# Kernel optimization log

Measured on AMD Instinct MI355X. Metric: run time of the kernel, lower is better.

## Reference

```python
import jax, jax.numpy as jnp
from jax import lax
import numpy as np

NUM_GRIDS = (40, 36, 24, 16, 12)
B, C = 4, 256
SMPL_OUT, CATE_OUT = 157, 1  # 24*6 pose + 10 shape + 3 cam; num_classes-1
SIZES = ((200, 200), (100, 100), (50, 50), (25, 25), (13, 13))


def setup_inputs():
    key = jax.random.key(0)
    ks = jax.random.split(key, 16)
    inp = {}
    for i, (h, w) in enumerate(SIZES):
        inp['feat%d' % i] = jax.random.normal(ks[i], (B, C, h, w), jnp.float32)
    def W(k, shape):
        return jax.random.normal(k, shape, jnp.float32) * 0.02
    inp['smpl_w0'] = W(ks[5], (C, C + 2, 3, 3)); inp['smpl_b0'] = jnp.zeros((C,), jnp.float32)
    inp['smpl_w'] = W(ks[6], (3, C, C, 3, 3)); inp['smpl_b'] = jnp.zeros((3, C), jnp.float32)
    inp['cate_w0'] = W(ks[7], (C, C, 3, 3)); inp['cate_b0'] = jnp.zeros((C,), jnp.float32)
    inp['cate_w'] = W(ks[8], (3, C, C, 3, 3)); inp['cate_b'] = jnp.zeros((3, C), jnp.float32)
    inp['cate_head_w'] = W(ks[9], (CATE_OUT, C, 3, 3)); inp['cate_head_b'] = jnp.zeros((CATE_OUT,), jnp.float32)
    inp['smpl_head_w'] = W(ks[10], (SMPL_OUT, C, 1, 1)); inp['smpl_head_b'] = jnp.zeros((SMPL_OUT,), jnp.float32)
    inp['smpl_init'] = W(ks[11], (SMPL_OUT,))  # stands in for init_contrep/shape/cam buffer
    return inp


def conv2d(x, w, b, pad):
    y = lax.conv_general_dilated(x, w, (1, 1), [(pad, pad), (pad, pad)],
                                 dimension_numbers=('NCHW', 'OIHW', 'NCHW'))
    return y + b[None, :, None, None]


def resize_ac(x, oh, ow):
    # bilinear resize, align_corners=True (matches F.interpolate(..., align_corners=True))
    H, W = x.shape[-2], x.shape[-1]
    ys = jnp.linspace(0.0, H - 1.0, oh)
    xs = jnp.linspace(0.0, W - 1.0, ow)
    y0 = jnp.floor(ys).astype(jnp.int32); y1 = jnp.minimum(y0 + 1, H - 1)
    x0 = jnp.floor(xs).astype(jnp.int32); x1 = jnp.minimum(x0 + 1, W - 1)
    wy = (ys - y0)[:, None]; wx = xs - x0
    r0, r1 = x[..., y0, :], x[..., y1, :]
    top = r0[..., x0] * (1 - wx) + r0[..., x1] * wx
    bot = r1[..., x0] * (1 - wx) + r1[..., x1] * wx
    return top * (1 - wy) + bot * wy


def points_nms(heat):
    # max_pool2d(kernel=2, stride=1, pad=1) -> (H+1, W+1); compare on [:-1, :-1]
    hmax = lax.reduce_window(heat, -jnp.inf, lax.max, (1, 1, 2, 2), (1, 1, 1, 1),
                             [(0, 0), (0, 0), (1, 1), (1, 1)])[:, :, :-1, :-1]
    return heat * (hmax == heat).astype(heat.dtype)


def _forward(feats, p):
    # split_feats: downsample P2 by 0.5, upsample P6 to P5 size (both align_corners bilinear)
    f0 = resize_ac(feats[0], feats[0].shape[-2] // 2, feats[0].shape[-1] // 2)
    f4 = resize_ac(feats[4], feats[3].shape[-2], feats[3].shape[-1])
    new_feats = (f0, feats[1], feats[2], feats[3], f4)
    smpl_outs, cate_outs = [], []
    for idx, x in enumerate(new_feats):
        g = NUM_GRIDS[idx]
        b, _, h, w = x.shape
        xr = jnp.linspace(-1.0, 1.0, w); yr = jnp.linspace(-1.0, 1.0, h)
        yy, xx = jnp.meshgrid(yr, xr, indexing='ij')
        coord = jnp.broadcast_to(jnp.stack([xx, yy])[None], (b, 2, h, w))  # CoordConv
        smpl_feat = resize_ac(jnp.concatenate([x, coord], axis=1), g, g)
        cate_feat = resize_ac(x, g, g)
        smpl_feat = jax.nn.relu(conv2d(smpl_feat, p['smpl_w0'], p['smpl_b0'], 1))
        cate_feat = jax.nn.relu(conv2d(cate_feat, p['cate_w0'], p['cate_b0'], 1))
        for i in range(3):  # remaining stacked convs (weights shared across levels)
            smpl_feat = jax.nn.relu(conv2d(smpl_feat, p['smpl_w'][i], p['smpl_b'][i], 1))
            cate_feat = jax.nn.relu(conv2d(cate_feat, p['cate_w'][i], p['cate_b'][i], 1))
        cate_pred = conv2d(cate_feat, p['cate_head_w'], p['cate_head_b'], 1)
        smpl_pred = conv2d(smpl_feat, p['smpl_head_w'], p['smpl_head_b'], 0) \
                    + p['smpl_init'][None, :, None, None]
        # eval=True branch: points-NMS on sigmoid heatmap, NHWC permute
        cate_pred = points_nms(jax.nn.sigmoid(cate_pred)).transpose(0, 2, 3, 1)
        smpl_pred = smpl_pred.transpose(0, 2, 3, 1)
        smpl_outs.append(smpl_pred); cate_outs.append(cate_pred)
    return tuple(smpl_outs) + tuple(cate_outs)


def reference(feat0, feat1, feat2, feat3, feat4, smpl_w0, smpl_b0, smpl_w, smpl_b,
              cate_w0, cate_b0, cate_w, cate_b, cate_head_w, cate_head_b,
              smpl_head_w, smpl_head_b, smpl_init):
    p = dict(smpl_w0=smpl_w0, smpl_b0=smpl_b0, smpl_w=smpl_w, smpl_b=smpl_b,
             cate_w0=cate_w0, cate_b0=cate_b0, cate_w=cate_w, cate_b=cate_b,
             cate_head_w=cate_head_w, cate_head_b=cate_head_b,
             smpl_head_w=smpl_head_w, smpl_head_b=smpl_head_b, smpl_init=smpl_init)
    return _forward((feat0, feat1, feat2, feat3, feat4), p)
```

## Files before the change

kernel.cpp:

```cpp
#include <hip/hip_runtime.h>
#include <math.h>
#include <stdint.h>

#define NLEV 5
#define PPT 17616

typedef __attribute__((ext_vector_type(8))) __bf16 bf16x8;
typedef __attribute__((ext_vector_type(4))) float f32x4;
typedef unsigned int u32;
typedef unsigned short u16;

__device__ __forceinline__ u32 f2bf(float f) {
  u32 u = __builtin_bit_cast(u32, f);
  return (u + 0x7FFFu + ((u >> 16) & 1u)) >> 16;
}
__device__ __forceinline__ u32 packSplit(float v) {
  u32 hi = f2bf(v);
  float fhi = __builtin_bit_cast(float, hi << 16);
  u32 lo = f2bf(v - fhi);
  return hi | (lo << 16);
}
__device__ __forceinline__ float unpackSum(u32 w) {
  return __builtin_bit_cast(float, w << 16) +
         __builtin_bit_cast(float, w & 0xFFFF0000u);
}


struct PrepDesc {
  const float* src[8];
  int Cin[8];
  int CB[8];
  int dstOff[8];
};

__global__ __launch_bounds__(256) void prep_weights(PrepDesc pd, u16* __restrict__ wHi,
                                                    u16* __restrict__ wLo) {
  int cfg = blockIdx.y;
  int CB = pd.CB[cfg];
  int KS = CB * 9;
  int total = KS * 8192;
  int didx = blockIdx.x * 256 + threadIdx.x;
  if (didx >= total) return;
  int j = didx & 7;
  int lane = (didx >> 3) & 63;
  int wco = (didx >> 9) & 1;
  int f = (didx >> 10) & 1;
  int rest = didx >> 11;
  int ks = rest % KS;
  int coT = rest / KS;
  int cb = ks / 9;
  int tap = ks - cb * 9;
  int ci = cb * 32 + ((lane >> 4) << 3) + j;
  int co = coT * 64 + wco * 32 + f * 16 + (lane & 15);
  int Cin = pd.Cin[cfg];
  float v = 0.f;
  if (ci < Cin) v = pd.src[cfg][((size_t)co * Cin + ci) * 9 + tap];
  u32 hi = f2bf(v);
  float fhi = __builtin_bit_cast(float, hi << 16);
  u32 lo = f2bf(v - fhi);
  wHi[pd.dstOff[cfg] + didx] = (u16)hi;
  wLo[pd.dstOff[cfg] + didx] = (u16)lo;
}

struct BuildDesc {
  const float* src[NLEV];
  int H[NLEV];
  int mid[NLEV];
  int P[NLEV];
  int g[NLEV];
  int padOff[NLEV];
};

__device__ __forceinline__ float bsample(const float* __restrict__ pl, int H, int W,
                                         float fy, float fx) {
  int y0 = (int)floorf(fy);
  int y1 = min(y0 + 1, H - 1);
  float wy = fy - (float)y0;
  int x0 = (int)floorf(fx);
  int x1 = min(x0 + 1, W - 1);
  float wx = fx - (float)x0;
  const float* r0 = pl + (size_t)y0 * W;
  const float* r1 = pl + (size_t)y1 * W;
  float top = r0[x0] * (1.f - wx) + r0[x1] * wx;
  float bot = r1[x0] * (1.f - wx) + r1[x1] * wx;
// ... 35 lines not shown
      float wy = fym - (float)y0;
      int x0 = (int)floorf(fxm);
      int x1 = min(x0 + 1, midw - 1);
      float wx = fxm - (float)x0;
      float sy0 = (float)y0 * (float)(H - 1) / (float)(midh - 1);
      float sy1 = (float)y1 * (float)(H - 1) / (float)(midh - 1);
      float sx0 = (float)x0 * (float)(W - 1) / (float)(midw - 1);
      float sx1 = (float)x1 * (float)(W - 1) / (float)(midw - 1);
      float v00 = bsample(pl, H, W, sy0, sx0);
      float v01 = bsample(pl, H, W, sy0, sx1);
      float v10 = bsample(pl, H, W, sy1, sx0);
      float v11 = bsample(pl, H, W, sy1, sx1);
      float top = v00 * (1.f - wx) + v01 * wx;
      float bot = v10 * (1.f - wx) + v11 * wx;
      val = top * (1.f - wy) + bot * wy;
    }
  }
  int gp2 = g + 2;
  int hpos = bd.padOff[l] + b * gp2 * gp2 + (i + 1) * gp2 + (j + 1);
  dst[((size_t)(c >> 3) * PPT + hpos) * 8 + (c & 7)] = packSplit(val);
}

struct ConvDesc {
  int tileStart[NLEV + 1];
  int padOff[NLEV];
  int g[NLEV];
};

#define HPX 240

__global__ __launch_bounds__(256) void conv_mfma(
    const u32* __restrict__ actIn, const u16* __restrict__ wHi,
    const u16* __restrict__ wLo, const float* __restrict__ bias,
    u32* __restrict__ actOut, ConvDesc d, int CB) {
  const int bid = blockIdx.x;
  const int xcd = bid & 7;
  const int i6 = bid >> 3;
  const int coT = i6 & 3;
  const int tile = xcd + (i6 >> 2) * 8;
  const int NT = d.tileStart[NLEV];
  if (tile >= NT) return;

  int l = 0;
#pragma unroll
  for (int i = 1; i < NLEV; i++)
    if (tile >= d.tileStart[i]) l = i;
  const int g = d.g[l];
  const int gp2 = g + 2;
  const int hp2 = gp2 * gp2;
  const int gg = g * g;
  const int padOff = d.padOff[l];
  const int t = threadIdx.x;
  const int lane = t & 63;
  const int wv = t >> 6;
  const int wco = wv & 1, wp = wv >> 1;
  const int KS = CB * 9;
  const int ptile = (tile - d.tileStart[l]) * 64;

  int b0 = ptile / gg;
  int pr0 = ptile - b0 * gg;
  int y0p = pr0 / g;
  int x0p = pr0 - y0p * g;
  const int h0 = padOff + b0 * hp2 + (y0p + 1) * gp2 + (x0p + 1) - gp2 - 1;

  const int pF0 = ptile + wp * 32 + (lane & 15);
  int bF = pF0 / gg;
  int prF = pF0 - bF * gg;
  int yF = prF / g;
  int xF = prF - yF * g;
  const int hF0 = padOff + bF * hp2 + (yF + 1) * gp2 + (xF + 1);
  int pF1 = pF0 + 16;
  int bF1 = pF1 / gg;
  int prF1 = pF1 - bF1 * gg;
  int yF1 = prF1 / g;
  int xF1 = prF1 - yF1 * g;
  const int hF1 = padOff + bF1 * hp2 + (yF1 + 1) * gp2 + (xF1 + 1);

  const int kb = lane >> 4;
  const int base0 = (hF0 - h0) * 4 + kb * (2 * HPX * 4);
  const int base1 = (hF1 - h0) * 4 + kb * (2 * HPX * 4);

  __shared__ u32 halo[4 * 2 * HPX * 4];

  const int sgr = t >> 6;
  const int spx = t & 63;

  f32x4 acc00 = {0.f, 0.f, 0.f, 0.f}, acc01 = {0.f, 0.f, 0.f, 0.f};
  f32x4 acc10 = {0.f, 0.f, 0.f, 0.f}, acc11 = {0.f, 0.f, 0.f, 0.f};

  const size_t wbase =
      (size_t)coT * KS * 2048 + (size_t)wco * 512 + (size_t)lane * 8;
  bf16x8 ah0 = *(const bf16x8*)(wHi + wbase);
  bf16x8 ah1 = *(const bf16x8*)(wHi + wbase + 1024);
  bf16x8 al0 = *(const bf16x8*)(wLo + wbase);
  bf16x8 al1 = *(const bf16x8*)(wLo + wbase + 1024);

  for (int cb = 0; cb < CB; ++cb) {
    __syncthreads();
    {
      int gr = cb * 4 + sgr;
      const u32* srcp = actIn + ((size_t)gr * PPT + h0 + spx) * 8;
#pragma unroll
      for (int i = 0; i < 4; i++) {
        int idx = i * 64 + spx;
        uint4 a = *(const uint4*)(srcp + (size_t)i * 512);
        uint4 b2 = *(const uint4*)(srcp + (size_t)i * 512 + 4);
        if (idx < HPX) {
          *(uint4*)(halo + sgr * (2 * HPX * 4) + idx * 4) = a;
          *(uint4*)(halo + sgr * (2 * HPX * 4) + HPX * 4 + idx * 4) = b2;
        }
      }
    }
    __syncthreads();

#pragma unroll
    for (int tap = 0; tap < 9; ++tap) {
      const int ks = cb * 9 + tap;
      bf16x8 ah0n, ah1n, al0n, al1n;
      const bool have = (ks + 1) < KS;
      if (have) {
        size_t wo = wbase + (size_t)(ks + 1) * 2048;
        ah0n = *(const bf16x8*)(wHi + wo);
        ah1n = *(const bf16x8*)(wHi + wo + 1024);
        al0n = *(const bf16x8*)(wLo + wo);
        al1n = *(const bf16x8*)(wLo + wo + 1024);
      }
      const int toff = (tap / 3 - 1) * gp2 + (tap % 3) - 1;
      const u32* hp0 = halo + base0 + toff * 4;
      uint4 q0 = *(const uint4*)hp0;
      uint4 q1 = *(const uint4*)(hp0 + HPX * 4);
      const u32* hp1 = halo + base1 + toff * 4;
      uint4 r0 = *(const uint4*)hp1;
      uint4 r1 = *(const uint4*)(hp1 + HPX * 4);

      bf16x8 bh0, bl0, bh1, bl1;
      {
        uint4 hq, lq;
        hq.x = __builtin_amdgcn_perm(q0.y, q0.x, 0x05040100u);
        hq.y = __builtin_amdgcn_perm(q0.w, q0.z, 0x05040100u);
        hq.z = __builtin_amdgcn_perm(q1.y, q1.x, 0x05040100u);
        hq.w = __builtin_amdgcn_perm(q1.w, q1.z, 0x05040100u);
        lq.x = __builtin_amdgcn_perm(q0.y, q0.x, 0x07060302u);
        lq.y = __builtin_amdgcn_perm(q0.w, q0.z, 0x07060302u);
        lq.z = __builtin_amdgcn_perm(q1.y, q1.x, 0x07060302u);
        lq.w = __builtin_amdgcn_perm(q1.w, q1.z, 0x07060302u);
        bh0 = __builtin_bit_cast(bf16x8, hq);
        bl0 = __builtin_bit_cast(bf16x8, lq);
        hq.x = __builtin_amdgcn_perm(r0.y, r0.x, 0x05040100u);
        hq.y = __builtin_amdgcn_perm(r0.w, r0.z, 0x05040100u);
        hq.z = __builtin_amdgcn_perm(r1.y, r1.x, 0x05040100u);
        hq.w = __builtin_amdgcn_perm(r1.w, r1.z, 0x05040100u);
        lq.x = __builtin_amdgcn_perm(r0.y, r0.x, 0x07060302u);
        lq.y = __builtin_amdgcn_perm(r0.w, r0.z, 0x07060302u);
        lq.z = __builtin_amdgcn_perm(r1.y, r1.x, 0x07060302u);
        lq.w = __builtin_amdgcn_perm(r1.w, r1.z, 0x07060302u);
        bh1 = __builtin_bit_cast(bf16x8, hq);
        bl1 = __builtin_bit_cast(bf16x8, lq);
      }

      acc00 = __builtin_amdgcn_mfma_f32_16x16x32_bf16(ah0, bh0, acc00, 0, 0, 0);
      acc00 = __builtin_amdgcn_mfma_f32_16x16x32_bf16(ah0, bl0, acc00, 0, 0, 0);
      acc00 = __builtin_amdgcn_mfma_f32_16x16x32_bf16(al0, bh0, acc00, 0, 0, 0);
      acc01 = __builtin_amdgcn_mfma_f32_16x16x32_bf16(ah0, bh1, acc01, 0, 0, 0);
      acc01 = __builtin_amdgcn_mfma_f32_16x16x32_bf16(ah0, bl1, acc01, 0, 0, 0);
      acc01 = __builtin_amdgcn_mfma_f32_16x16x32_bf16(al0, bh1, acc01, 0, 0, 0);
      acc10 = __builtin_amdgcn_mfma_f32_16x16x32_bf16(ah1, bh0, acc10, 0, 0, 0);
      acc10 = __builtin_amdgcn_mfma_f32_16x16x32_bf16(ah1, bl0, acc10, 0, 0, 0);
      acc10 = __builtin_amdgcn_mfma_f32_16x16x32_bf16(al1, bh0, acc10, 0, 0, 0);
      acc11 = __builtin_amdgcn_mfma_f32_16x16x32_bf16(ah1, bh1, acc11, 0, 0, 0);
      acc11 = __builtin_amdgcn_mfma_f32_16x16x32_bf16(ah1, bl1, acc11, 0, 0, 0);
      acc11 = __builtin_amdgcn_mfma_f32_16x16x32_bf16(al1, bh1, acc11, 0, 0, 0);
      if (have) {
        ah0 = ah0n;
        ah1 = ah1n;
        al0 = al0n;
        al1 = al1n;
      }
    }
  }

  int obase[2];
#pragma unroll
  for (int fp = 0; fp < 2; ++fp) {
    int po = ptile + wp * 32 + fp * 16 + (lane & 15);
    int bb = po / gg;
    int prr = po - bb * gg;
    int yy = prr / g;
    int xx = prr - yy * g;
    obase[fp] = padOff + bb * hp2 + (yy + 1) * gp2 + (xx + 1);
  }
  const int coBase = coT * 64 + wco * 32 + ((lane >> 4) << 2);
  float4 bA = *(const float4*)(bias + coBase);
  float4 bB = *(const float4*)(bias + coBase + 16);
  const size_t rowA = (size_t)(coBase >> 3) * PPT;
  const size_t rowB = (size_t)((coBase + 16) >> 3) * PPT;
  const int sub = coBase & 7;
  uint4 s;
  s.x = packSplit(fmaxf(acc00[0] + bA.x, 0.f));
  s.y = packSplit(fmaxf(acc00[1] + bA.y, 0.f));
  s.z = packSplit(fmaxf(acc00[2] + bA.z, 0.f));
  s.w = packSplit(fmaxf(acc00[3] + bA.w, 0.f));
  *(uint4*)(actOut + (rowA + obase[0]) * 8 + sub) = s;
  s.x = packSplit(fmaxf(acc01[0] + bA.x, 0.f));
  s.y = packSplit(fmaxf(acc01[1] + bA.y, 0.f));
  s.z = packSplit(fmaxf(acc01[2] + bA.z, 0.f));
  s.w = packSplit(fmaxf(acc01[3] + bA.w, 0.f));
  *(uint4*)(actOut + (rowA + obase[1]) * 8 + sub) = s;
  s.x = packSplit(fmaxf(acc10[0] + bB.x, 0.f));
  s.y = packSplit(fmaxf(acc10[1] + bB.y, 0.f));
  s.z = packSplit(fmaxf(acc10[2] + bB.z, 0.f));
  s.w = packSplit(fmaxf(acc10[3] + bB.w, 0.f));
  *(uint4*)(actOut + (rowB + obase[0]) * 8 + sub) = s;
  s.x = packSplit(fmaxf(acc11[0] + bB.x, 0.f));
  s.y = packSplit(fmaxf(acc11[1] + bB.y, 0.f));
  s.z = packSplit(fmaxf(acc11[2] + bB.z, 0.f));
  s.w = packSplit(fmaxf(acc11[3] + bB.w, 0.f));
  *(uint4*)(actOut + (rowB + obase[1]) * 8 + sub) = s;
}

struct HeadDesc {
  int tileStart[NLEV + 1];
  int padOff[NLEV];
  int g[NLEV];
  int outOff[NLEV];
};

__global__ __launch_bounds__(256) void head1x1(
    const u32* __restrict__ actIn, const float* __restrict__ w,
    const float* __restrict__ bias, const float* __restrict__ bias2,
    float* __restrict__ outB, HeadDesc d) {
  int bx = blockIdx.x;
  int l = 0;
#pragma unroll
  for (int i = 1; i < NLEV; i++)
    if (bx >= d.tileStart[i]) l = i;
  const int g = d.g[l];
  const int gp2 = g + 2, hp2 = gp2 * gp2, gg = g * g;
  const int t = threadIdx.x;
  const int ptile = (bx - d.tileStart[l]) * 64;
  const int pp = t & 63;
  int p = ptile + pp;
  int b = p / gg, pr = p - b * gg, y = pr / g, x = pr - y * g;
  const int hbase = d.padOff[l] + b * hp2 + (y + 1) * gp2 + (x + 1);
  const int co_tile = blockIdx.y * 64;
  __shared__ float As[32][68];
  __shared__ float Bs[32][68];
  const int tx = t & 15, ty = t >> 4;
  const int akk = t & 31, aco = t >> 5;
  const int kg = t >> 6;
  float acc[4][4];
#pragma unroll
  for (int i = 0; i < 4; i++)
#pragma unroll
    for (int j = 0; j < 4; j++) acc[i][j] = 0.f;

  for (int k0 = 0; k0 < 256; k0 += 32) {
#pragma unroll
    for (int i = 0; i < 8; i++) {
      int co = i * 8 + aco;
      int coG = co_tile + co;
      As[akk][co] = (coG < 157) ? w[(size_t)coG * 256 + k0 + akk] : 0.f;
    }
    {
      const u32* src = actIn + (((size_t)(k0 >> 3) + kg) * PPT + hbase) * 8;
#pragma unroll
      for (int j = 0; j < 8; j++) Bs[kg * 8 + j][pp] = unpackSum(src[j]);
    }
    __syncthreads();
#pragma unroll
    for (int kk = 0; kk < 32; kk++) {
      float4 a4 = *reinterpret_cast<const float4*>(&As[kk][ty * 4]);
      float4 b4 = *reinterpret_cast<const float4*>(&Bs[kk][tx * 4]);
      float av[4] = {a4.x, a4.y, a4.z, a4.w};
      float bv[4] = {b4.x, b4.y, b4.z, b4.w};
#pragma unroll
      for (int i = 0; i < 4; i++)
#pragma unroll
        for (int j = 0; j < 4; j++) acc[i][j] = fmaf(av[i], bv[j], acc[i][j]);
    }
    __syncthreads();
  }
  const int co0 = co_tile + ty * 4;
#pragma unroll
  for (int i = 0; i < 4; i++) {
    int co = co0 + i;
    if (co < 157) {
      float bb = bias[co] + bias2[co];
#pragma unroll
      for (int j = 0; j < 4; j++) {
        int pg = ptile + tx * 4 + j;
        outB[d.outOff[l] + (size_t)pg * 157 + co] = acc[i][j] + bb;
      }
    }
  }
}

struct CHDesc {
  int tileStart[NLEV + 1];
  int padOff[NLEV];
  int g[NLEV];
  int outOff[NLEV];
};

__global__ __launch_bounds__(256) void cate_head_all(
    const u32* __restrict__ actIn, const float* __restrict__ w,
    const float* __restrict__ bias, float* __restrict__ heat, CHDesc d) {
  int tile = blockIdx.x;
  int l = 0;
#pragma unroll
  for (int i = 1; i < NLEV; i++)
    if (tile >= d.tileStart[i]) l = i;
  const int g = d.g[l];
  const int gp2 = g + 2, hp2 = gp2 * gp2, gg = g * g;
  const int t = threadIdx.x;
  const int ps = t & 63;
  const int cw = t >> 6;
  const int ptile = (tile - d.tileStart[l]) * 64;
  int p = ptile + ps;
  int b = p / gg, pr = p - b * gg, y = pr / g, x = pr - y * g;
  const int hbase = d.padOff[l] + b * hp2 + (y + 1) * gp2 + (x + 1);

  __shared__ float ws[32][9][8];
  for (int i = t; i < 2304; i += 256) {
    int ci = i / 9, tap = i - ci * 9;
    ws[ci >> 3][tap][ci & 7] = w[i];
  }
  __syncthreads();

  float s = 0.f;
  for (int gr = cw; gr < 32; gr += 4) {
    const u32* bp = actIn + ((size_t)gr * PPT + hbase) * 8;
#pragma unroll
    for (int tap = 0; tap < 9; tap++) {
      const int toff = (tap / 3 - 1) * gp2 + (tap % 3) - 1;
      uint4 q0 = *(const uint4*)(bp + (ptrdiff_t)toff * 8);
      uint4 q1 = *(const uint4*)(bp + (ptrdiff_t)toff * 8 + 4);
      const float* wp = ws[gr][tap];
      s += unpackSum(q0.x) * wp[0] + unpackSum(q0.y) * wp[1] +
           unpackSum(q0.z) * wp[2] + unpackSum(q0.w) * wp[3] +
           unpackSum(q1.x) * wp[4] + unpackSum(q1.y) * wp[5] +
// ... 40 lines not shown
                              void* d_out, int out_size, void* d_ws, size_t ws_size,
                              hipStream_t stream) {
  const float* feat[5];
  for (int i = 0; i < 5; i++) feat[i] = (const float*)d_in[i];
  const float* smpl_w0 = (const float*)d_in[5];
  const float* smpl_b0 = (const float*)d_in[6];
  const float* smpl_w = (const float*)d_in[7];
  const float* smpl_b = (const float*)d_in[8];
  const float* cate_w0 = (const float*)d_in[9];
  const float* cate_b0 = (const float*)d_in[10];
  const float* cate_w = (const float*)d_in[11];
  const float* cate_b = (const float*)d_in[12];
  const float* cate_head_w = (const float*)d_in[13];
  const float* cate_head_b = (const float*)d_in[14];
  const float* smpl_head_w = (const float*)d_in[15];
  const float* smpl_head_b = (const float*)d_in[16];
  const float* smpl_init = (const float*)d_in[17];
  float* out = (float*)d_out;

  static const int GR[5] = {40, 36, 24, 16, 12};
  static const int SH[5] = {200, 100, 50, 25, 13};
  static const int MIDW[5] = {100, 0, 0, 0, 25};

  int P[5], cumP[6], tS[6], padOff[5];
  cumP[0] = 0;
  tS[0] = 0;
  int po = 0;
  for (int l = 0; l < 5; l++) {
    P[l] = 4 * GR[l] * GR[l];
    cumP[l + 1] = cumP[l] + P[l];
    tS[l + 1] = tS[l] + P[l] / 64;
    padOff[l] = po;
    po += 4 * (GR[l] + 2) * (GR[l] + 2);
  }

  int smpl_off[5], cate_off[5];
  {
    int off = 0;
    for (int l = 0; l < 5; l++) {
      smpl_off[l] = off;
      off += P[l] * 157;
    }
    for (int l = 0; l < 5; l++) {
      cate_off[l] = off;
      off += P[l];
    }
  }

  u32* bufA = (u32*)d_ws;
  u32* bufB = bufA + (size_t)33 * PPT * 8;
  u32* bufC = bufB + (size_t)32 * PPT * 8;
  float* heat = (float*)(bufC + (size_t)32 * PPT * 8);
  const size_t WTOT = (size_t)(81 + 7 * 72) * 8192;
  u16* wHi = (u16*)(heat + 15488);
  u16* wLo = wHi + WTOT;
  const size_t ACT_BYTES = (size_t)(33 + 32 + 32) * PPT * 8 * 4 + 15488 * 4;

  hipMemsetAsync(d_ws, 0, ACT_BYTES, stream);

  PrepDesc pd;
  const size_t LSTR = (size_t)256 * 256 * 9;
  pd.src[0] = smpl_w0;  pd.Cin[0] = 258;  pd.CB[0] = 9;
  pd.src[1] = smpl_w;   pd.Cin[1] = 256;  pd.CB[1] = 8;
  pd.src[2] = smpl_w + LSTR;     pd.Cin[2] = 256; pd.CB[2] = 8;
  pd.src[3] = smpl_w + 2 * LSTR; pd.Cin[3] = 256; pd.CB[3] = 8;
  pd.src[4] = cate_w0;  pd.Cin[4] = 256;  pd.CB[4] = 8;
  pd.src[5] = cate_w;   pd.Cin[5] = 256;  pd.CB[5] = 8;
  pd.src[6] = cate_w + LSTR;     pd.Cin[6] = 256; pd.CB[6] = 8;
  pd.src[7] = cate_w + 2 * LSTR; pd.Cin[7] = 256; pd.CB[7] = 8;
  {
    int off = 0;
    for (int i = 0; i < 8; i++) {
      pd.dstOff[i] = off;
      off += pd.CB[i] * 9 * 8192;
    }
  }
  hipLaunchKernelGGL(prep_weights, dim3(81 * 32, 8), dim3(256), 0, stream, pd, wHi,
                     wLo);

  BuildDesc bd;
  for (int l = 0; l < 5; l++) {
    bd.src[l] = feat[l];
    bd.H[l] = SH[l];
    bd.mid[l] = MIDW[l];
    bd.P[l] = P[l];
    bd.g[l] = GR[l];
    bd.padOff[l] = padOff[l];
  }
  hipLaunchKernelGGL(build_all, dim3((258 * P[0] + 255) / 256, 5), dim3(256), 0,
                     stream, bd, bufA);

  ConvDesc cd;
  HeadDesc hd;
  CHDesc chd;
  SmallDesc nd;
  for (int i = 0; i <= 5; i++) {
    cd.tileStart[i] = tS[i];
    hd.tileStart[i] = tS[i];
    chd.tileStart[i] = tS[i];
  }
  for (int l = 0; l < 5; l++) {
    cd.padOff[l] = padOff[l];
    cd.g[l] = GR[l];
    hd.padOff[l] = padOff[l];
    hd.g[l] = GR[l];
    hd.outOff[l] = smpl_off[l];
    chd.padOff[l] = padOff[l];
    chd.g[l] = GR[l];
    chd.outOff[l] = cumP[l];
    nd.P[l] = P[l];
    nd.g[l] = GR[l];
    nd.inOff[l] = cumP[l];
    nd.outOff[l] = cate_off[l];
  }

  const int NT = tS[5];
  const int CGRID = 8 * 124;
  hipLaunchKernelGGL(conv_mfma, dim3(CGRID), dim3(256), 0, stream, bufA,
                     wHi + pd.dstOff[0], wLo + pd.dstOff[0], smpl_b0, bufB, cd, 9);
  hipLaunchKernelGGL(conv_mfma, dim3(CGRID), dim3(256), 0, stream, bufB,
                     wHi + pd.dstOff[1], wLo + pd.dstOff[1], smpl_b + 0, bufC, cd, 8);
  hipLaunchKernelGGL(conv_mfma, dim3(CGRID), dim3(256), 0, stream, bufC,
                     wHi + pd.dstOff[2], wLo + pd.dstOff[2], smpl_b + 256, bufB, cd,
                     8);
  hipLaunchKernelGGL(conv_mfma, dim3(CGRID), dim3(256), 0, stream, bufB,
                     wHi + pd.dstOff[3], wLo + pd.dstOff[3], smpl_b + 512, bufC, cd,
                     8);
  hipLaunchKernelGGL(head1x1, dim3(NT, 3), dim3(256), 0, stream, bufC, smpl_head_w,
                     smpl_head_b, smpl_init, out, hd);
  hipLaunchKernelGGL(conv_mfma, dim3(CGRID), dim3(256), 0, stream, bufA,
                     wHi + pd.dstOff[4], wLo + pd.dstOff[4], cate_b0, bufB, cd, 8);
  hipLaunchKernelGGL(conv_mfma, dim3(CGRID), dim3(256), 0, stream, bufB,
                     wHi + pd.dstOff[5], wLo + pd.dstOff[5], cate_b + 0, bufC, cd, 8);
  hipLaunchKernelGGL(conv_mfma, dim3(CGRID), dim3(256), 0, stream, bufC,
                     wHi + pd.dstOff[6], wLo + pd.dstOff[6], cate_b + 256, bufB, cd,
                     8);
  hipLaunchKernelGGL(conv_mfma, dim3(CGRID), dim3(256), 0, stream, bufB,
                     wHi + pd.dstOff[7], wLo + pd.dstOff[7], cate_b + 512, bufC, cd,
                     8);
  hipLaunchKernelGGL(cate_head_all, dim3(NT), dim3(256), 0, stream, bufC,
                     cate_head_w, cate_head_b, heat, chd);
  hipLaunchKernelGGL(nms_all, dim3((P[0] + 255) / 256, 5), dim3(256), 0, stream,
                     heat, out, nd);
  (void)in_sizes;
  (void)n_in;
  (void)out_size;
  (void)ws_size;
}
```

Baseline: 607.8 us.

## Merge smpl/cate conv towers per launch, widen pixel tiles, MFMA 1x1 head

Each conv launch now runs both the smpl and cate towers, with the tower picked by block index, so eight conv launches become four larger ones. Pixel tiles grow from 64 to 128 per block with four fragments per wave, and the hi/lo split permutation moves into the halo staging step so each tap reads bf16 operands straight from LDS. The 1x1 smpl head moves from a scalar FMA GEMM to MFMA with pre-split weights. The full-buffer memset is replaced by a kernel that zeroes only halo borders. The larger tiles raise register and LDS use and add tail masking for partial tiles.

```diff
diff --git a/kernel.cpp b/kernel.cpp
--- a/kernel.cpp
+++ b/kernel.cpp
@@ -4,11 +4,14 @@
 
 #define NLEV 5
 #define PPT 17616
+#define HPX 320
 
 typedef __attribute__((ext_vector_type(8))) __bf16 bf16x8;
 typedef __attribute__((ext_vector_type(4))) float f32x4;
 typedef unsigned int u32;
 typedef unsigned short u16;
+
+#define MFMA16 __builtin_amdgcn_mfma_f32_16x16x32_bf16
 
 __device__ __forceinline__ u32 f2bf(float f) {
   u32 u = __builtin_bit_cast(u32, f);
@@ -24,21 +27,36 @@
   return __builtin_bit_cast(float, w << 16) +
          __builtin_bit_cast(float, w & 0xFFFF0000u);
 }
+__device__ __forceinline__ void splitPerm(const uint4& a, const uint4& b, uint4& hq,
+                                          uint4& lq) {
+  hq.x = __builtin_amdgcn_perm(a.y, a.x, 0x05040100u);
+  hq.y = __builtin_amdgcn_perm(a.w, a.z, 0x05040100u);
+  hq.z = __builtin_amdgcn_perm(b.y, b.x, 0x05040100u);
+  hq.w = __builtin_amdgcn_perm(b.w, b.z, 0x05040100u);
+  lq.x = __builtin_amdgcn_perm(a.y, a.x, 0x07060302u);
+  lq.y = __builtin_amdgcn_perm(a.w, a.z, 0x07060302u);
+  lq.z = __builtin_amdgcn_perm(b.y, b.x, 0x07060302u);
+  lq.w = __builtin_amdgcn_perm(b.w, b.z, 0x07060302u);
+}
 
 
 struct PrepDesc {
-  const float* src[8];
-  int Cin[8];
-  int CB[8];
-  int dstOff[8];
+  const float* src[9];
+  int Cin[9];
+  int Cout[9];
+  int CB[9];
+  int TAPS[9];
+  int nCoT[9];
+  int dstOff[9];
 };
 
 __global__ __launch_bounds__(256) void prep_weights(PrepDesc pd, u16* __restrict__ wHi,
                                                     u16* __restrict__ wLo) {
   int cfg = blockIdx.y;
   int CB = pd.CB[cfg];
-  int KS = CB * 9;
-  int total = KS * 8192;
+  int TAPS = pd.TAPS[cfg];
+  int KS = CB * TAPS;
+  int total = KS * 2048 * pd.nCoT[cfg];
   int didx = blockIdx.x * 256 + threadIdx.x;
   if (didx >= total) return;
   int j = didx & 7;
@@ -48,18 +66,43 @@
   int rest = didx >> 11;
   int ks = rest % KS;
   int coT = rest / KS;
-  int cb = ks / 9;
-  int tap = ks - cb * 9;
+  int cb = ks / TAPS;
+  int tap = ks - cb * TAPS;
   int ci = cb * 32 + ((lane >> 4) << 3) + j;
   int co = coT * 64 + wco * 32 + f * 16 + (lane & 15);
-  int Cin = pd.Cin[cfg];
   float v = 0.f;
-  if (ci < Cin) v = pd.src[cfg][((size_t)co * Cin + ci) * 9 + tap];
+  if (ci < pd.Cin[cfg] && co < pd.Cout[cfg])
+    v = pd.src[cfg][((size_t)co * pd.Cin[cfg] + ci) * TAPS + tap];
   u32 hi = f2bf(v);
   float fhi = __builtin_bit_cast(float, hi << 16);
   u32 lo = f2bf(v - fhi);
   wHi[pd.dstOff[cfg] + didx] = (u16)hi;
   wLo[pd.dstOff[cfg] + didx] = (u16)lo;
+}
+
+struct ZeroDesc {
+  int padOff[NLEV];
+  int g[NLEV];
+};
+
+__global__ __launch_bounds__(256) void halo_zero(u32* __restrict__ base, ZeroDesc zd) {
+  int px = blockIdx.x * 256 + threadIdx.x;
+  if (px >= PPT) return;
+  int l = 0;
+#pragma unroll
+  for (int i = 1; i < NLEV; i++)
+    if (px >= zd.padOff[i]) l = i;
+  int g = zd.g[l], gp2 = g + 2, hp2 = gp2 * gp2;
+  int local = px - zd.padOff[l];
+  int b = local / hp2;
+  int rem = local - b * hp2;
+  int yy = rem / gp2, xx = rem - yy * gp2;
+  if (yy >= 1 && yy <= g && xx >= 1 && xx <= g) return;
+  int r = blockIdx.y;
+  uint4 z = {0u, 0u, 0u, 0u};
+  u32* p = base + ((size_t)r * PPT + px) * 8;
+  *(uint4*)p = z;
+  *(uint4*)(p + 4) = z;
 }
 
 struct BuildDesc {
@@ -141,93 +184,104 @@
 }
 
 struct ConvDesc {
-  int tileStart[NLEV + 1];
+  int tS[NLEV + 1];
   int padOff[NLEV];
   int g[NLEV];
+  int P[NLEV];
 };
 
-#define HPX 240
-
 __global__ __launch_bounds__(256) void conv_mfma(
-    const u32* __restrict__ actIn, const u16* __restrict__ wHi,
-    const u16* __restrict__ wLo, const float* __restrict__ bias,
-    u32* __restrict__ actOut, ConvDesc d, int CB) {
+    const u32* __restrict__ inS, const u32* __restrict__ inC,
+    const u16* __restrict__ wHiB, const u16* __restrict__ wLoB, int wOffS,
+    int wOffC, const float* __restrict__ bS, const float* __restrict__ bC,
+    u32* __restrict__ outS, u32* __restrict__ outC, ConvDesc d, int CBS, int CBC) {
   const int bid = blockIdx.x;
   const int xcd = bid & 7;
   const int i6 = bid >> 3;
-  const int coT = i6 & 3;
-  const int tile = xcd + (i6 >> 2) * 8;
-  const int NT = d.tileStart[NLEV];
-  if (tile >= NT) return;
+  const int tower = i6 & 1;
+  const int coT = (i6 >> 1) & 3;
+  const int tile = xcd + (i6 >> 3) * 8;
+  if (tile >= d.tS[NLEV]) return;
+
+  const u32* __restrict__ actIn = tower ? inC : inS;
+  u32* __restrict__ actOut = tower ? outC : outS;
+  const u16* __restrict__ wH = wHiB + (tower ? wOffC : wOffS);
+  const u16* __restrict__ wL = wLoB + (tower ? wOffC : wOffS);
+  const float* __restrict__ bias = tower ? bC : bS;
+  const int CB = tower ? CBC : CBS;
+  const int KS = CB * 9;
 
   int l = 0;
 #pragma unroll
   for (int i = 1; i < NLEV; i++)
-    if (tile >= d.tileStart[i]) l = i;
+    if (tile >= d.tS[i]) l = i;
   const int g = d.g[l];
-  const int gp2 = g + 2;
-  const int hp2 = gp2 * gp2;
-  const int gg = g * g;
+  const int gp2 = g + 2, hp2 = gp2 * gp2, gg = g * g;
   const int padOff = d.padOff[l];
+  const int Pl = d.P[l];
+  const int ptile = (tile - d.tS[l]) * 128;
+
   const int t = threadIdx.x;
   const int lane = t & 63;
   const int wv = t >> 6;
   const int wco = wv & 1, wp = wv >> 1;
-  const int KS = CB * 9;
-  const int ptile = (tile - d.tileStart[l]) * 64;
-
-  int b0 = ptile / gg;
-  int pr0 = ptile - b0 * gg;
-  int y0p = pr0 / g;
-  int x0p = pr0 - y0p * g;
-  const int h0 = padOff + b0 * hp2 + (y0p + 1) * gp2 + (x0p + 1) - gp2 - 1;
-
-  const int pF0 = ptile + wp * 32 + (lane & 15);
-  int bF = pF0 / gg;
-  int prF = pF0 - bF * gg;
-  int yF = prF / g;
-  int xF = prF - yF * g;
-  const int hF0 = padOff + bF * hp2 + (yF + 1) * gp2 + (xF + 1);
-  int pF1 = pF0 + 16;
-  int bF1 = pF1 / gg;
-  int prF1 = pF1 - bF1 * gg;
-  int yF1 = prF1 / g;
-  int xF1 = prF1 - yF1 * g;
-  const int hF1 = padOff + bF1 * hp2 + (yF1 + 1) * gp2 + (xF1 + 1);
-
   const int kb = lane >> 4;
-  const int base0 = (hF0 - h0) * 4 + kb * (2 * HPX * 4);
-  const int base1 = (hF1 - h0) * 4 + kb * (2 * HPX * 4);
+  const int sgr = wv;
+  const int spx = lane;
+
+  int h0;
+  {
+    int b0 = ptile / gg, pr0 = ptile - b0 * gg;
+    int y0 = pr0 / g, x0 = pr0 - y0 * g;
+    h0 = padOff + b0 * hp2 + (y0 + 1) * gp2 + (x0 + 1) - gp2 - 1;
+  }
+
+  int hRel[4], ob[4];
+  bool vst[4];
+#pragma unroll
+  for (int fi = 0; fi < 4; fi++) {
+    int pb = ptile + wp * 64 + fi * 16;
+    vst[fi] = pb < Pl;
+    int pf = pb + (lane & 15);
+    if (pf >= Pl) pf = Pl - 1;
+    int b = pf / gg, pr = pf - b * gg;
+    int y = pr / g, x = pr - y * g;
+    int h = padOff + b * hp2 + (y + 1) * gp2 + (x + 1);
+    hRel[fi] = h - h0;
+    ob[fi] = h;
+  }
 
   __shared__ u32 halo[4 * 2 * HPX * 4];
 
-  const int sgr = t >> 6;
-  const int spx = t & 63;
-
-  f32x4 acc00 = {0.f, 0.f, 0.f, 0.f}, acc01 = {0.f, 0.f, 0.f, 0.f};
-  f32x4 acc10 = {0.f, 0.f, 0.f, 0.f}, acc11 = {0.f, 0.f, 0.f, 0.f};
+  f32x4 acc[2][4];
+#pragma unroll
+  for (int c = 0; c < 2; c++)
+#pragma unroll
+    for (int fi = 0; fi < 4; fi++) acc[c][fi] = (f32x4){0.f, 0.f, 0.f, 0.f};
 
   const size_t wbase =
       (size_t)coT * KS * 2048 + (size_t)wco * 512 + (size_t)lane * 8;
-  bf16x8 ah0 = *(const bf16x8*)(wHi + wbase);
-  bf16x8 ah1 = *(const bf16x8*)(wHi + wbase + 1024);
-  bf16x8 al0 = *(const bf16x8*)(wLo + wbase);
-  bf16x8 al1 = *(const bf16x8*)(wLo + wbase + 1024);
+  bf16x8 ah0 = *(const bf16x8*)(wH + wbase);
+  bf16x8 ah1 = *(const bf16x8*)(wH + wbase + 1024);
+  bf16x8 al0 = *(const bf16x8*)(wL + wbase);
+  bf16x8 al1 = *(const bf16x8*)(wL + wbase + 1024);
 
   for (int cb = 0; cb < CB; ++cb) {
     __syncthreads();
     {
-      int gr = cb * 4 + sgr;
-      const u32* srcp = actIn + ((size_t)gr * PPT + h0 + spx) * 8;
-#pragma unroll
-      for (int i = 0; i < 4; i++) {
-        int idx = i * 64 + spx;
-        uint4 a = *(const uint4*)(srcp + (size_t)i * 512);
-        uint4 b2 = *(const uint4*)(srcp + (size_t)i * 512 + 4);
-        if (idx < HPX) {
-          *(uint4*)(halo + sgr * (2 * HPX * 4) + idx * 4) = a;
-          *(uint4*)(halo + sgr * (2 * HPX * 4) + HPX * 4 + idx * 4) = b2;
-        }
+      const int gr = cb * 4 + sgr;
+      const u32* srcp = actIn + ((size_t)gr * PPT + h0) * 8;
+      u32* dhi = halo + sgr * (2 * HPX * 4);
+      u32* dlo = dhi + HPX * 4;
+#pragma unroll
+      for (int i = 0; i < 5; i++) {
+        int px = i * 64 + spx;
+        uint4 a = *(const uint4*)(srcp + (size_t)px * 8);
+        uint4 b2 = *(const uint4*)(srcp + (size_t)px * 8 + 4);
+        uint4 hq, lq;
+        splitPerm(a, b2, hq, lq);
+        *(uint4*)(dhi + px * 4) = hq;
+        *(uint4*)(dlo + px * 4) = lq;
       }
     }
     __syncthreads();
@@ -239,56 +293,25 @@
       const bool have = (ks + 1) < KS;
       if (have) {
         size_t wo = wbase + (size_t)(ks + 1) * 2048;
-        ah0n = *(const bf16x8*)(wHi + wo);
-        ah1n = *(const bf16x8*)(wHi + wo + 1024);
-        al0n = *(const bf16x8*)(wLo + wo);
-        al1n = *(const bf16x8*)(wLo + wo + 1024);
+        ah0n = *(const bf16x8*)(wH + wo);
+        ah1n = *(const bf16x8*)(wH + wo + 1024);
+        al0n = *(const bf16x8*)(wL + wo);
+        al1n = *(const bf16x8*)(wL + wo + 1024);
       }
       const int toff = (tap / 3 - 1) * gp2 + (tap % 3) - 1;
-      const u32* hp0 = halo + base0 + toff * 4;
-      uint4 q0 = *(const uint4*)hp0;
-      uint4 q1 = *(const uint4*)(hp0 + HPX * 4);
-      const u32* hp1 = halo + base1 + toff * 4;
-      uint4 r0 = *(const uint4*)hp1;
-      uint4 r1 = *(const uint4*)(hp1 + HPX * 4);
-
-      bf16x8 bh0, bl0, bh1, bl1;
-      {
-        uint4 hq, lq;
-        hq.x = __builtin_amdgcn_perm(q0.y, q0.x, 0x05040100u);
-        hq.y = __builtin_amdgcn_perm(q0.w, q0.z, 0x05040100u);
-        hq.z = __builtin_amdgcn_perm(q1.y, q1.x, 0x05040100u);
-        hq.w = __builtin_amdgcn_perm(q1.w, q1.z, 0x05040100u);
-        lq.x = __builtin_amdgcn_perm(q0.y, q0.x, 0x07060302u);
-        lq.y = __builtin_amdgcn_perm(q0.w, q0.z, 0x07060302u);
-        lq.z = __builtin_amdgcn_perm(q1.y, q1.x, 0x07060302u);
-        lq.w = __builtin_amdgcn_perm(q1.w, q1.z, 0x07060302u);
-        bh0 = __builtin_bit_cast(bf16x8, hq);
-        bl0 = __builtin_bit_cast(bf16x8, lq);
-        hq.x = __builtin_amdgcn_perm(r0.y, r0.x, 0x05040100u);
-        hq.y = __builtin_amdgcn_perm(r0.w, r0.z, 0x05040100u);
-        hq.z = __builtin_amdgcn_perm(r1.y, r1.x, 0x05040100u);
-        hq.w = __builtin_amdgcn_perm(r1.w, r1.z, 0x05040100u);
-        lq.x = __builtin_amdgcn_perm(r0.y, r0.x, 0x07060302u);
-        lq.y = __builtin_amdgcn_perm(r0.w, r0.z, 0x07060302u);
-        lq.z = __builtin_amdgcn_perm(r1.y, r1.x, 0x07060302u);
-        lq.w = __builtin_amdgcn_perm(r1.w, r1.z, 0x07060302u);
-        bh1 = __builtin_bit_cast(bf16x8, hq);
-        bl1 = __builtin_bit_cast(bf16x8, lq);
+      const u32* kbase = halo + kb * (2 * HPX * 4);
+#pragma unroll
+      for (int fi = 0; fi < 4; fi++) {
+        const u32* p0 = kbase + (hRel[fi] + toff) * 4;
+        bf16x8 bh = __builtin_bit_cast(bf16x8, *(const uint4*)p0);
+        bf16x8 bl = __builtin_bit_cast(bf16x8, *(const uint4*)(p0 + HPX * 4));
+        acc[0][fi] = MFMA16(ah0, bh, acc[0][fi], 0, 0, 0);
+        acc[0][fi] = MFMA16(ah0, bl, acc[0][fi], 0, 0, 0);
+        acc[0][fi] = MFMA16(al0, bh, acc[0][fi], 0, 0, 0);
+        acc[1][fi] = MFMA16(ah1, bh, acc[1][fi], 0, 0, 0);
+        acc[1][fi] = MFMA16(ah1, bl, acc[1][fi], 0, 0, 0);
+        acc[1][fi] = MFMA16(al1, bh, acc[1][fi], 0, 0, 0);
       }
-
-      acc00 = __builtin_amdgcn_mfma_f32_16x16x32_bf16(ah0, bh0, acc00, 0, 0, 0);
-      acc00 = __builtin_amdgcn_mfma_f32_16x16x32_bf16(ah0, bl0, acc00, 0, 0, 0);
-      acc00 = __builtin_amdgcn_mfma_f32_16x16x32_bf16(al0, bh0, acc00, 0, 0, 0);
-      acc01 = __builtin_amdgcn_mfma_f32_16x16x32_bf16(ah0, bh1, acc01, 0, 0, 0);
-      acc01 = __builtin_amdgcn_mfma_f32_16x16x32_bf16(ah0, bl1, acc01, 0, 0, 0);
-      acc01 = __builtin_amdgcn_mfma_f32_16x16x32_bf16(al0, bh1, acc01, 0, 0, 0);
-      acc10 = __builtin_amdgcn_mfma_f32_16x16x32_bf16(ah1, bh0, acc10, 0, 0, 0);
-      acc10 = __builtin_amdgcn_mfma_f32_16x16x32_bf16(ah1, bl0, acc10, 0, 0, 0);
-      acc10 = __builtin_amdgcn_mfma_f32_16x16x32_bf16(al1, bh0, acc10, 0, 0, 0);
-      acc11 = __builtin_amdgcn_mfma_f32_16x16x32_bf16(ah1, bh1, acc11, 0, 0, 0);
-      acc11 = __builtin_amdgcn_mfma_f32_16x16x32_bf16(ah1, bl1, acc11, 0, 0, 0);
-      acc11 = __builtin_amdgcn_mfma_f32_16x16x32_bf16(al1, bh1, acc11, 0, 0, 0);
       if (have) {
         ah0 = ah0n;
         ah1 = ah1n;
@@ -298,124 +321,106 @@
     }
   }
 
-  int obase[2];
-#pragma unroll
-  for (int fp = 0; fp < 2; ++fp) {
-    int po = ptile + wp * 32 + fp * 16 + (lane & 15);
-    int bb = po / gg;
-    int prr = po - bb * gg;
-    int yy = prr / g;
-    int xx = prr - yy * g;
-    obase[fp] = padOff + bb * hp2 + (yy + 1) * gp2 + (xx + 1);
-  }
   const int coBase = coT * 64 + wco * 32 + ((lane >> 4) << 2);
   float4 bA = *(const float4*)(bias + coBase);
   float4 bB = *(const float4*)(bias + coBase + 16);
   const size_t rowA = (size_t)(coBase >> 3) * PPT;
   const size_t rowB = (size_t)((coBase + 16) >> 3) * PPT;
   const int sub = coBase & 7;
-  uint4 s;
-  s.x = packSplit(fmaxf(acc00[0] + bA.x, 0.f));
-  s.y = packSplit(fmaxf(acc00[1] + bA.y, 0.f));
-  s.z = packSplit(fmaxf(acc00[2] + bA.z, 0.f));
-  s.w = packSplit(fmaxf(acc00[3] + bA.w, 0.f));
-  *(uint4*)(actOut + (rowA + obase[0]) * 8 + sub) = s;
-  s.x = packSplit(fmaxf(acc01[0] + bA.x, 0.f));
-  s.y = packSplit(fmaxf(acc01[1] + bA.y, 0.f));
-  s.z = packSplit(fmaxf(acc01[2] + bA.z, 0.f));
-  s.w = packSplit(fmaxf(acc01[3] + bA.w, 0.f));
-  *(uint4*)(actOut + (rowA + obase[1]) * 8 + sub) = s;
-  s.x = packSplit(fmaxf(acc10[0] + bB.x, 0.f));
-  s.y = packSplit(fmaxf(acc10[1] + bB.y, 0.f));
-  s.z = packSplit(fmaxf(acc10[2] + bB.z, 0.f));
-  s.w = packSplit(fmaxf(acc10[3] + bB.w, 0.f));
-  *(uint4*)(actOut + (rowB + obase[0]) * 8 + sub) = s;
-  s.x = packSplit(fmaxf(acc11[0] + bB.x, 0.f));
-  s.y = packSplit(fmaxf(acc11[1] + bB.y, 0.f));
-  s.z = packSplit(fmaxf(acc11[2] + bB.z, 0.f));
-  s.w = packSplit(fmaxf(acc11[3] + bB.w, 0.f));
-  *(uint4*)(actOut + (rowB + obase[1]) * 8 + sub) = s;
+#pragma unroll
+  for (int fi = 0; fi < 4; fi++) {
+    if (!vst[fi]) continue;
+    uint4 s;
+    s.x = packSplit(fmaxf(acc[0][fi][0] + bA.x, 0.f));
+    s.y = packSplit(fmaxf(acc[0][fi][1] + bA.y, 0.f));
+    s.z = packSplit(fmaxf(acc[0][fi][2] + bA.z, 0.f));
+    s.w = packSplit(fmaxf(acc[0][fi][3] + bA.w, 0.f));
+    *(uint4*)(actOut + (rowA + ob[fi]) * 8 + sub) = s;
+    s.x = packSplit(fmaxf(acc[1][fi][0] + bB.x, 0.f));
+    s.y = packSplit(fmaxf(acc[1][fi][1] + bB.y, 0.f));
+    s.z = packSplit(fmaxf(acc[1][fi][2] + bB.z, 0.f));
+    s.w = packSplit(fmaxf(acc[1][fi][3] + bB.w, 0.f));
+    *(uint4*)(actOut + (rowB + ob[fi]) * 8 + sub) = s;
+  }
 }
 
 struct HeadDesc {
-  int tileStart[NLEV + 1];
+  int tS64[NLEV + 1];
   int padOff[NLEV];
   int g[NLEV];
   int outOff[NLEV];
 };
 
 __global__ __launch_bounds__(256) void head1x1(
-    const u32* __restrict__ actIn, const float* __restrict__ w,
-    const float* __restrict__ bias, const float* __restrict__ bias2,
-    float* __restrict__ outB, HeadDesc d) {
-  int bx = blockIdx.x;
+    const u32* __restrict__ actIn, const u16* __restrict__ wH,
+    const u16* __restrict__ wL, const float* __restrict__ bias,
+    const float* __restrict__ bias2, float* __restrict__ outB, HeadDesc d) {
+  const int bx = blockIdx.x;
+  const int coT = blockIdx.y;
   int l = 0;
 #pragma unroll
   for (int i = 1; i < NLEV; i++)
-    if (bx >= d.tileStart[i]) l = i;
-  const int g = d.g[l];
-  const int gp2 = g + 2, hp2 = gp2 * gp2, gg = g * g;
-  const int t = threadIdx.x;
-  const int ptile = (bx - d.tileStart[l]) * 64;
-  const int pp = t & 63;
-  int p = ptile + pp;
-  int b = p / gg, pr = p - b * gg, y = pr / g, x = pr - y * g;
-  const int hbase = d.padOff[l] + b * hp2 + (y + 1) * gp2 + (x + 1);
-  const int co_tile = blockIdx.y * 64;
-  __shared__ float As[32][68];
-  __shared__ float Bs[32][68];
-  const int tx = t & 15, ty = t >> 4;
-  const int akk = t & 31, aco = t >> 5;
-  const int kg = t >> 6;
-  float acc[4][4];
-#pragma unroll
-  for (int i = 0; i < 4; i++)
-#pragma unroll
-    for (int j = 0; j < 4; j++) acc[i][j] = 0.f;
-
-  for (int k0 = 0; k0 < 256; k0 += 32) {
-#pragma unroll
-    for (int i = 0; i < 8; i++) {
-      int co = i * 8 + aco;
-      int coG = co_tile + co;
-      As[akk][co] = (coG < 157) ? w[(size_t)coG * 256 + k0 + akk] : 0.f;
+    if (bx >= d.tS64[i]) l = i;
+  const int g = d.g[l], gp2 = g + 2, hp2 = gp2 * gp2, gg = g * g;
+  const int ptile = (bx - d.tS64[l]) * 64;
+  const int t = threadIdx.x, lane = t & 63, wv = t >> 6;
+  const int wco = wv & 1, wp = wv >> 1, kb = lane >> 4;
+
+  int hp[2], pF[2];
+#pragma unroll
+  for (int fi = 0; fi < 2; fi++) {
+    int pf = ptile + wp * 32 + fi * 16 + (lane & 15);
+    pF[fi] = pf;
+    int b = pf / gg, pr = pf - b * gg, y = pr / g, x = pr - y * g;
+    hp[fi] = d.padOff[l] + b * hp2 + (y + 1) * gp2 + (x + 1);
+  }
+  f32x4 acc[2][2];
+#pragma unroll
+  for (int c = 0; c < 2; c++)
+#pragma unroll
+    for (int fi = 0; fi < 2; fi++) acc[c][fi] = (f32x4){0.f, 0.f, 0.f, 0.f};
+
+  const size_t wbase = (size_t)coT * 8 * 2048 + (size_t)wco * 512 + (size_t)lane * 8;
+  for (int cb = 0; cb < 8; ++cb) {
+    size_t wo = wbase + (size_t)cb * 2048;
+    bf16x8 ah0 = *(const bf16x8*)(wH + wo);
+    bf16x8 ah1 = *(const bf16x8*)(wH + wo + 1024);
+    bf16x8 al0 = *(const bf16x8*)(wL + wo);
+    bf16x8 al1 = *(const bf16x8*)(wL + wo + 1024);
+    const int gr = cb * 4 + kb;
+#pragma unroll
+    for (int fi = 0; fi < 2; fi++) {
+      const u32* bp = actIn + ((size_t)gr * PPT + hp[fi]) * 8;
+      uint4 a = *(const uint4*)bp;
+      uint4 b2 = *(const uint4*)(bp + 4);
+      uint4 hq, lq;
+      splitPerm(a, b2, hq, lq);
+      bf16x8 bh = __builtin_bit_cast(bf16x8, hq);
+      bf16x8 bl = __builtin_bit_cast(bf16x8, lq);
+      acc[0][fi] = MFMA16(ah0, bh, acc[0][fi], 0, 0, 0);
+      acc[0][fi] = MFMA16(ah0, bl, acc[0][fi], 0, 0, 0);
+      acc[0][fi] = MFMA16(al0, bh, acc[0][fi], 0, 0, 0);
+      acc[1][fi] = MFMA16(ah1, bh, acc[1][fi], 0, 0, 0);
+      acc[1][fi] = MFMA16(ah1, bl, acc[1][fi], 0, 0, 0);
+      acc[1][fi] = MFMA16(al1, bh, acc[1][fi], 0, 0, 0);
     }
-    {
-      const u32* src = actIn + (((size_t)(k0 >> 3) + kg) * PPT + hbase) * 8;
-#pragma unroll
-      for (int j = 0; j < 8; j++) Bs[kg * 8 + j][pp] = unpackSum(src[j]);
-    }
-    __syncthreads();
-#pragma unroll
-    for (int kk = 0; kk < 32; kk++) {
-      float4 a4 = *reinterpret_cast<const float4*>(&As[kk][ty * 4]);
-      float4 b4 = *reinterpret_cast<const float4*>(&Bs[kk][tx * 4]);
-      float av[4] = {a4.x, a4.y, a4.z, a4.w};
-      float bv[4] = {b4.x, b4.y, b4.z, b4.w};
-#pragma unroll
-      for (int i = 0; i < 4; i++)
-#pragma unroll
-        for (int j = 0; j < 4; j++) acc[i][j] = fmaf(av[i], bv[j], acc[i][j]);
-    }
-    __syncthreads();
-  }
-  const int co0 = co_tile + ty * 4;
-#pragma unroll
-  for (int i = 0; i < 4; i++) {
-    int co = co0 + i;
-    if (co < 157) {
-      float bb = bias[co] + bias2[co];
-#pragma unroll
-      for (int j = 0; j < 4; j++) {
-        int pg = ptile + tx * 4 + j;
-        outB[d.outOff[l] + (size_t)pg * 157 + co] = acc[i][j] + bb;
+  }
+  const int coBase = coT * 64 + wco * 32 + ((lane >> 4) << 2);
+#pragma unroll
+  for (int c = 0; c < 2; c++)
+#pragma unroll
+    for (int fi = 0; fi < 2; fi++)
+#pragma unroll
+      for (int i = 0; i < 4; i++) {
+        int co = coBase + c * 16 + i;
+        if (co < 157)
+          outB[d.outOff[l] + (size_t)pF[fi] * 157 + co] =
+              acc[c][fi][i] + bias[co] + bias2[co];
       }
-    }
-  }
 }
 
 struct CHDesc {
-  int tileStart[NLEV + 1];
+  int tS64[NLEV + 1];
   int padOff[NLEV];
   int g[NLEV];
   int outOff[NLEV];
@@ -428,13 +433,13 @@
   int l = 0;
 #pragma unroll
   for (int i = 1; i < NLEV; i++)
-    if (tile >= d.tileStart[i]) l = i;
+    if (tile >= d.tS64[i]) l = i;
   const int g = d.g[l];
   const int gp2 = g + 2, hp2 = gp2 * gp2, gg = g * g;
   const int t = threadIdx.x;
   const int ps = t & 63;
   const int cw = t >> 6;
-  const int ptile = (tile - d.tileStart[l]) * 64;
+  const int ptile = (tile - d.tS64[l]) * 64;
   int p = ptile + ps;
   int b = p / gg, pr = p - b * gg, y = pr / g, x = pr - y * g;
   const int hbase = d.padOff[l] + b * hp2 + (y + 1) * gp2 + (x + 1);
@@ -521,14 +526,16 @@
   static const int SH[5] = {200, 100, 50, 25, 13};
   static const int MIDW[5] = {100, 0, 0, 0, 25};
 
-  int P[5], cumP[6], tS[6], padOff[5];
+  int P[5], cumP[6], tS64[6], tS128[6], padOff[5];
   cumP[0] = 0;
-  tS[0] = 0;
+  tS64[0] = 0;
+  tS128[0] = 0;
   int po = 0;
   for (int l = 0; l < 5; l++) {
     P[l] = 4 * GR[l] * GR[l];
     cumP[l + 1] = cumP[l] + P[l];
-    tS[l + 1] = tS[l] + P[l] / 64;
+    tS64[l + 1] = tS64[l] + P[l] / 64;
+    tS128[l + 1] = tS128[l] + (P[l] + 127) / 128;
     padOff[l] = po;
     po += 4 * (GR[l] + 2) * (GR[l] + 2);
   }
@@ -547,35 +554,53 @@
   }
 
   u32* bufA = (u32*)d_ws;
-  u32* bufB = bufA + (size_t)33 * PPT * 8;
-  u32* bufC = bufB + (size_t)32 * PPT * 8;
-  float* heat = (float*)(bufC + (size_t)32 * PPT * 8);
-  const size_t WTOT = (size_t)(81 + 7 * 72) * 8192;
+  u32* bufBs = bufA + (size_t)36 * PPT * 8;
+  u32* bufCs = bufBs + (size_t)32 * PPT * 8;
+  u32* bufBc = bufCs + (size_t)32 * PPT * 8;
+  u32* bufCc = bufBc + (size_t)32 * PPT * 8;
+  float* heat = (float*)(bufCc + (size_t)32 * PPT * 8);
   u16* wHi = (u16*)(heat + 15488);
-  u16* wLo = wHi + WTOT;
-  const size_t ACT_BYTES = (size_t)(33 + 32 + 32) * PPT * 8 * 4 + 15488 * 4;
-
-  hipMemsetAsync(d_ws, 0, ACT_BYTES, stream);
 
   PrepDesc pd;
   const size_t LSTR = (size_t)256 * 256 * 9;
-  pd.src[0] = smpl_w0;  pd.Cin[0] = 258;  pd.CB[0] = 9;
-  pd.src[1] = smpl_w;   pd.Cin[1] = 256;  pd.CB[1] = 8;
-  pd.src[2] = smpl_w + LSTR;     pd.Cin[2] = 256; pd.CB[2] = 8;
-  pd.src[3] = smpl_w + 2 * LSTR; pd.Cin[3] = 256; pd.CB[3] = 8;
-  pd.src[4] = cate_w0;  pd.Cin[4] = 256;  pd.CB[4] = 8;
-  pd.src[5] = cate_w;   pd.Cin[5] = 256;  pd.CB[5] = 8;
-  pd.src[6] = cate_w + LSTR;     pd.Cin[6] = 256; pd.CB[6] = 8;
-  pd.src[7] = cate_w + 2 * LSTR; pd.Cin[7] = 256; pd.CB[7] = 8;
-  {
-    int off = 0;
-    for (int i = 0; i < 8; i++) {
-      pd.dstOff[i] = off;
-      off += pd.CB[i] * 9 * 8192;
-    }
-  }
-  hipLaunchKernelGGL(prep_weights, dim3(81 * 32, 8), dim3(256), 0, stream, pd, wHi,
-                     wLo);
+  pd.src[0] = smpl_w0;
+  pd.src[1] = smpl_w;
+  pd.src[2] = smpl_w + LSTR;
+  pd.src[3] = smpl_w + 2 * LSTR;
+  pd.src[4] = cate_w0;
+  pd.src[5] = cate_w;
+  pd.src[6] = cate_w + LSTR;
+  pd.src[7] = cate_w + 2 * LSTR;
+  pd.src[8] = smpl_head_w;
+  for (int i = 0; i < 9; i++) {
+    pd.Cin[i] = 256;
+    pd.Cout[i] = 256;
+    pd.CB[i] = 8;
+    pd.TAPS[i] = 9;
+    pd.nCoT[i] = 4;
+  }
+  pd.Cin[0] = 258;
+  pd.CB[0] = 9;
+  pd.Cout[8] = 157;
+  pd.TAPS[8] = 1;
+  pd.nCoT[8] = 3;
+  size_t WTOT = 0;
+  for (int i = 0; i < 9; i++) {
+    pd.dstOff[i] = (int)WTOT;
+    WTOT += (size_t)pd.CB[i] * pd.TAPS[i] * 2048 * pd.nCoT[i];
+  }
+  u16* wLo = wHi + WTOT;
+
+  hipMemsetAsync(bufA, 0, (size_t)36 * PPT * 32, stream);
+  ZeroDesc zd;
+  for (int l = 0; l < 5; l++) {
+    zd.padOff[l] = padOff[l];
+    zd.g[l] = GR[l];
+  }
+  hipLaunchKernelGGL(halo_zero, dim3((PPT + 255) / 256, 128), dim3(256), 0, stream,
+                     bufBs, zd);
+
+  hipLaunchKernelGGL(prep_weights, dim3(2592, 9), dim3(256), 0, stream, pd, wHi, wLo);
 
   BuildDesc bd;
   for (int l = 0; l < 5; l++) {
@@ -594,13 +619,14 @@
   CHDesc chd;
   SmallDesc nd;
   for (int i = 0; i <= 5; i++) {
-    cd.tileStart[i] = tS[i];
-    hd.tileStart[i] = tS[i];
-    chd.tileStart[i] = tS[i];
+    cd.tS[i] = tS128[i];
+    hd.tS64[i] = tS64[i];
+    chd.tS64[i] = tS64[i];
   }
   for (int l = 0; l < 5; l++) {
     cd.padOff[l] = padOff[l];
     cd.g[l] = GR[l];
+    cd.P[l] = P[l];
     hd.padOff[l] = padOff[l];
     hd.g[l] = GR[l];
     hd.outOff[l] = smpl_off[l];
@@ -613,34 +639,27 @@
     nd.outOff[l] = cate_off[l];
   }
 
-  const int NT = tS[5];
-  const int CGRID = 8 * 124;
-  hipLaunchKernelGGL(conv_mfma, dim3(CGRID), dim3(256), 0, stream, bufA,
-                     wHi + pd.dstOff[0], wLo + pd.dstOff[0], smpl_b0, bufB, cd, 9);
-  hipLaunchKernelGGL(conv_mfma, dim3(CGRID), dim3(256), 0, stream, bufB,
-                     wHi + pd.dstOff[1], wLo + pd.dstOff[1], smpl_b + 0, bufC, cd, 8);
-  hipLaunchKernelGGL(conv_mfma, dim3(CGRID), dim3(256), 0, stream, bufC,
-                     wHi + pd.dstOff[2], wLo + pd.dstOff[2], smpl_b + 256, bufB, cd,
-                     8);
-  hipLaunchKernelGGL(conv_mfma, dim3(CGRID), dim3(256), 0, stream, bufB,
-                     wHi + pd.dstOff[3], wLo + pd.dstOff[3], smpl_b + 512, bufC, cd,
-                     8);
-  hipLaunchKernelGGL(head1x1, dim3(NT, 3), dim3(256), 0, stream, bufC, smpl_head_w,
-                     smpl_head_b, smpl_init, out, hd);
-  hipLaunchKernelGGL(conv_mfma, dim3(CGRID), dim3(256), 0, stream, bufA,
-                     wHi + pd.dstOff[4], wLo + pd.dstOff[4], cate_b0, bufB, cd, 8);
-  hipLaunchKernelGGL(conv_mfma, dim3(CGRID), dim3(256), 0, stream, bufB,
-                     wHi + pd.dstOff[5], wLo + pd.dstOff[5], cate_b + 0, bufC, cd, 8);
-  hipLaunchKernelGGL(conv_mfma, dim3(CGRID), dim3(256), 0, stream, bufC,
-                     wHi + pd.dstOff[6], wLo + pd.dstOff[6], cate_b + 256, bufB, cd,
-                     8);
-  hipLaunchKernelGGL(conv_mfma, dim3(CGRID), dim3(256), 0, stream, bufB,
-                     wHi + pd.dstOff[7], wLo + pd.dstOff[7], cate_b + 512, bufC, cd,
-                     8);
-  hipLaunchKernelGGL(cate_head_all, dim3(NT), dim3(256), 0, stream, bufC,
+  const int NT64 = tS64[5];
+  const int CGRID = 8 * 128;
+  hipLaunchKernelGGL(conv_mfma, dim3(CGRID), dim3(256), 0, stream, bufA, bufA, wHi,
+                     wLo, pd.dstOff[0], pd.dstOff[4], smpl_b0, cate_b0, bufBs, bufBc,
+                     cd, 9, 8);
+  hipLaunchKernelGGL(conv_mfma, dim3(CGRID), dim3(256), 0, stream, bufBs, bufBc, wHi,
+                     wLo, pd.dstOff[1], pd.dstOff[5], smpl_b + 0, cate_b + 0, bufCs,
+                     bufCc, cd, 8, 8);
+  hipLaunchKernelGGL(conv_mfma, dim3(CGRID), dim3(256), 0, stream, bufCs, bufCc, wHi,
+                     wLo, pd.dstOff[2], pd.dstOff[6], smpl_b + 256, cate_b + 256,
+                     bufBs, bufBc, cd, 8, 8);
+  hipLaunchKernelGGL(conv_mfma, dim3(CGRID), dim3(256), 0, stream, bufBs, bufBc, wHi,
+                     wLo, pd.dstOff[3], pd.dstOff[7], smpl_b + 512, cate_b + 512,
+                     bufCs, bufCc, cd, 8, 8);
+  hipLaunchKernelGGL(head1x1, dim3(NT64, 3), dim3(256), 0, stream, bufCs,
+                     wHi + pd.dstOff[8], wLo + pd.dstOff[8], smpl_head_b, smpl_init,
+                     out, hd);
+  hipLaunchKernelGGL(cate_head_all, dim3(NT64), dim3(256), 0, stream, bufCc,
                      cate_head_w, cate_head_b, heat, chd);
-  hipLaunchKernelGGL(nms_all, dim3((P[0] + 255) / 256, 5), dim3(256), 0, stream,
-                     heat, out, nd);
+  hipLaunchKernelGGL(nms_all, dim3((P[0] + 255) / 256, 5), dim3(256), 0, stream, heat,
+                     out, nd);
   (void)in_sizes;
   (void)n_in;
   (void)out_size;
```

New measurement: 528.5 us. 1.15x faster.
